# Performance work log

Measured on AMD Instinct MI355X. Metric: run time of the kernel, lower is better.

The kernel has to match this reference:

```python
import jax, jax.numpy as jnp
import numpy as np

_SHAPE = (4, 2, 8, 256, 513)  # N, 2(real/imag), C, T, F


def setup_inputs() -> dict:
    key = jax.random.key(0)
    k1, k2, k3 = jax.random.split(key, 3)
    return {
        "mixture": jax.random.normal(k1, _SHAPE, dtype=jnp.float32),
        "target": jax.random.normal(k2, _SHAPE, dtype=jnp.float32),
        "noise": jax.random.normal(k3, _SHAPE, dtype=jnp.float32),
        "ref_mic_idx": 0,
    }


def _to_complex(x):
    # (N, 2, C, T, F) real-imag stacked -> complex (N, C, T, F)
    return jax.lax.complex(x[:, 0], x[:, 1])


def _mean_spatial_cov(s):
    # s: complex (N, C, T, F) -> time-averaged covariance (N, F, C, C)
    N, C, T, F = s.shape
    sc = jnp.transpose(s, (0, 3, 2, 1))  # (N, F, T, C)
    # outer product V V^H summed over T, fused into one batched GEMM
    return jnp.einsum("nftc,nftd->nfcd", sc, jnp.conj(sc)) / T


def reference(mixture, target, noise, ref_mic_idx):
    y = _to_complex(mixture)  # (N, C, T, F)
    x = _to_complex(target)
    v = _to_complex(noise)
    N, C, T, F = y.shape

    phi_target = _mean_spatial_cov(x)  # (N, F, C, C)
    # diagonal loading: torch adds load to BOTH real and imag parts (RI dim broadcast)
    load = (0.001 / np.sqrt(2)) * (1.0 + 1.0j)
    phi_noise = _mean_spatial_cov(v) + jnp.asarray(load, dtype=y.dtype) * jnp.eye(C, dtype=y.dtype)

    G = jnp.linalg.inv(phi_noise) @ phi_target  # (N, F, C, C)
    l = jnp.trace(G, axis1=-2, axis2=-1)  # (N, F)
    # W = (1/l) * G @ e_ref  -> select column ref_mic_idx
    W = G[..., ref_mic_idx] / l[..., None]  # (N, F, C)

    # X_bf(n,t,f) = W^H y = sum_c conj(W)_{nfc} y_{nctf}
    X_bf = jnp.einsum("nfc,nctf->ntf", jnp.conj(W), y)  # (N, T, F)
    # restack real/imag and add singleton channel dim -> (N, 2, 1, T, F)
    out = jnp.stack([X_bf.real, X_bf.imag], axis=1)[:, :, None]
    return out
```

## Files before the change

kernel.cpp:

```cpp
#include <hip/hip_runtime.h>

#define Nn 4
#define Cc 8
#define Tt 256
#define Ff 513
#define TFs (Tt * Ff)
#define NPAIR 36

template <int G>
__device__ __forceinline__ void cov_body(const float* __restrict__ base,
                                         float* __restrict__ dst,
                                         int t0, int tchunk)
{
    constexpr int R2 = 7 - G;
    float ar[9], ai[9];
#pragma unroll
    for (int s = 0; s < 9; ++s) { ar[s] = 0.f; ai[s] = 0.f; }

    const float* bt = base + (size_t)t0 * Ff;
    for (int tt = 0; tt < tchunk; ++tt) {
        float re[8], im[8];
#pragma unroll
        for (int c = G; c < 8; ++c) {
            re[c] = bt[(size_t)c * TFs];
            im[c] = bt[(size_t)(Cc + c) * TFs];
        }
        int s = 0;
#pragma unroll
        for (int d = G; d < 8; ++d, ++s) {
            ar[s] += re[G] * re[d] + im[G] * im[d];
            ai[s] += im[G] * re[d] - re[G] * im[d];
        }
#pragma unroll
        for (int d = R2; d < 8; ++d, ++s) {
            ar[s] += re[R2] * re[d] + im[R2] * im[d];
            ai[s] += im[R2] * re[d] - re[R2] * im[d];
        }
        bt += Ff;
    }

    int s = 0;
#pragma unroll
    for (int d = G; d < 8; ++d, ++s) {
        const int p = G * 8 - G * (G - 1) / 2 + (d - G);
        dst[(size_t)(p * 2 + 0) * Ff] = ar[s];
        dst[(size_t)(p * 2 + 1) * Ff] = ai[s];
    }
#pragma unroll
    for (int d = R2; d < 8; ++d, ++s) {
        const int p = R2 * 8 - R2 * (R2 - 1) / 2 + (d - R2);
        dst[(size_t)(p * 2 + 0) * Ff] = ar[s];
        dst[(size_t)(p * 2 + 1) * Ff] = ai[s];
    }
}

__global__ __launch_bounds__(64) void cov_partial(
    const float* __restrict__ target, const float* __restrict__ noise,
    float* __restrict__ partial, int nchunk, int tchunk)
{
    int f = blockIdx.x * 64 + threadIdx.x;
    if (f >= Ff) return;
    int n = blockIdx.y;
    int z = blockIdx.z;
    int g = z & 3;
    int inp = (z >> 2) & 1;
    int chunk = z >> 3;

    const float* src = inp ? noise : target;
    const float* base = src + (size_t)n * 2 * Cc * TFs + f;
    float* dst = partial +
        ((((size_t)inp * Nn + n) * nchunk + chunk) * (NPAIR * 2)) * Ff + f;
    int t0 = chunk * tchunk;

    switch (g) {
        case 0: cov_body<0>(base, dst, t0, tchunk); break;
        case 1: cov_body<1>(base, dst, t0, tchunk); break;
        case 2: cov_body<2>(base, dst, t0, tchunk); break;
        default: cov_body<3>(base, dst, t0, tchunk); break;
    }
}

__global__ __launch_bounds__(128) void mvdr_weights(
    const float* __restrict__ partial, const int* __restrict__ ref_ptr,
    float2* __restrict__ wconj, int nchunk)
{
    int f = blockIdx.x;
    int n = blockIdx.y;
    int tid = threadIdx.x;

    __shared__ float covT[72], covN[72];
    __shared__ float2 A[8][16];
    __shared__ float2 PT[8][8];
    __shared__ float2 gcol[8], trp[8];
    __shared__ int piv;

    if (tid < 72) {
        float sT = 0.f, sN = 0.f;
        for (int ch = 0; ch < nchunk; ++ch) {
            size_t iT = ((((size_t)0 * Nn + n) * nchunk + ch) * 72 + tid) * Ff + f;
            size_t iN = ((((size_t)1 * Nn + n) * nchunk + ch) * 72 + tid) * Ff + f;
            sT += partial[iT];
            sN += partial[iN];
        }
        covT[tid] = sT;
        covN[tid] = sN;
    }
    __syncthreads();

    const float invT = 1.0f / (float)Tt;
    const float dl = 0.001f / 1.41421356237309515f;

    if (tid < 64) {
        int r = tid >> 3, c = tid & 7;
        int lo = r <= c ? r : c, hi = r <= c ? c : r;
        int p = lo * 8 - lo * (lo - 1) / 2 + (hi - lo);
        float pr = covN[2 * p] * invT, pi = covN[2 * p + 1] * invT;
        if (r > c) pi = -pi;
        if (r == c) { pr += dl; pi += dl; }
        A[r][c] = make_float2(pr, pi);
        A[r][8 + c] = make_float2(r == c ? 1.f : 0.f, 0.f);
        float qr = covT[2 * p] * invT, qi = covT[2 * p + 1] * invT;
        if (r > c) qi = -qi;
        PT[r][c] = make_float2(qr, qi);
    }
    __syncthreads();

    int r = tid >> 4, col = tid & 15;
    for (int k = 0; k < 8; ++k) {
        if (tid == 0) {
            int best = k;
            float bm = A[k][k].x * A[k][k].x + A[k][k].y * A[k][k].y;
            for (int j = k + 1; j < 8; ++j) {
                float m = A[j][k].x * A[j][k].x + A[j][k].y * A[j][k].y;
                if (m > bm) { bm = m; best = j; }
            }
            piv = best;
        }
        __syncthreads();
        int pv_row = piv;
        if (pv_row != k && tid < 16) {
            float2 tmp = A[k][tid]; A[k][tid] = A[pv_row][tid]; A[pv_row][tid] = tmp;
        }
        __syncthreads();
        if (tid < 16) {
            float2 pv = A[k][k];
            float d = pv.x * pv.x + pv.y * pv.y;
            float2 ip = make_float2(pv.x / d, -pv.y / d);
            float2 a = A[k][tid];
            A[k][tid] = make_float2(a.x * ip.x - a.y * ip.y,
                                    a.x * ip.y + a.y * ip.x);
        }
        __syncthreads();
        float2 factor = A[r][k];
        float2 akc = A[k][col];
        if (r != k) {
            float2 v = A[r][col];
            A[r][col] = make_float2(v.x - (factor.x * akc.x - factor.y * akc.y),
                                    v.y - (factor.x * akc.y + factor.y * akc.x));
        }
        __syncthreads();
    }

    int ref = *ref_ptr;
    if (tid < 8) {
        float2 g = make_float2(0.f, 0.f), tr = make_float2(0.f, 0.f);
#pragma unroll
        for (int d = 0; d < 8; ++d) {
            float2 iv = A[tid][8 + d];
            float2 b = PT[d][ref];
            g.x += iv.x * b.x - iv.y * b.y;
            g.y += iv.x * b.y + iv.y * b.x;
            float2 b2 = PT[d][tid];
            tr.x += iv.x * b2.x - iv.y * b2.y;
            tr.y += iv.x * b2.y + iv.y * b2.x;
        }
        gcol[tid] = g; trp[tid] = tr;
    }
    __syncthreads();
    if (tid < 8) {
        float lx = 0.f, ly = 0.f;
#pragma unroll
        for (int j = 0; j < 8; ++j) { lx += trp[j].x; ly += trp[j].y; }
        float den = lx * lx + ly * ly;
        float2 g = gcol[tid];
        float wx = (g.x * lx + g.y * ly) / den;
        float wy = (g.y * lx - g.x * ly) / den;
        wconj[((size_t)n * Ff + f) * 8 + tid] = make_float2(wx, -wy);
    }
}

__global__ __launch_bounds__(256) void beamform(
    const float* __restrict__ y, const float2* __restrict__ wconj,
    float* __restrict__ out)
{
    int idx = blockIdx.x * 256 + threadIdx.x;
    int n = idx / TFs;
    int rem = idx - n * TFs;
    int t = rem / Ff;
    int f = rem - t * Ff;

    size_t base_re = (size_t)n * 2 * Cc * TFs + (size_t)t * Ff + f;
    size_t base_im = base_re + (size_t)Cc * TFs;
    const float2* w = wconj + ((size_t)n * Ff + f) * 8;

    float xr = 0.f, xi = 0.f;
#pragma unroll
    for (int c = 0; c < Cc; ++c) {
        float yre = y[base_re + (size_t)c * TFs];
        float yim = y[base_im + (size_t)c * TFs];
        float2 wc = w[c];
        xr += wc.x * yre - wc.y * yim;
        xi += wc.x * yim + wc.y * yre;
    }
    size_t ob = (size_t)n * 2 * TFs + (size_t)t * Ff + f;
    out[ob] = xr;
    out[ob + TFs] = xi;
}

extern "C" void kernel_launch(void* const* d_in, const int* in_sizes, int n_in,
                              void* d_out, int out_size, void* d_ws, size_t ws_size,
                              hipStream_t stream) {
    const float* mixture = (const float*)d_in[0];
    const float* target  = (const float*)d_in[1];
    const float* noise   = (const float*)d_in[2];
    const int*   refp    = (const int*)d_in[3];
    float* out = (float*)d_out;

    const size_t wconj_bytes = (size_t)Nn * Ff * 8 * sizeof(float2);
    int nchunk = 8;
    while (nchunk > 1 &&
           (size_t)2 * Nn * nchunk * 72 * Ff * sizeof(float) + wconj_bytes > ws_size)
        nchunk >>= 1;
    int tchunk = Tt / nchunk;

    float*  partial = (float*)d_ws;
    float2* wconj = (float2*)((char*)d_ws +
                              (size_t)2 * Nn * nchunk * 72 * Ff * sizeof(float));

    cov_partial<<<dim3(9, Nn, nchunk * 8), 64, 0, stream>>>(
        target, noise, partial, nchunk, tchunk);
    mvdr_weights<<<dim3(Ff, Nn), 128, 0, stream>>>(partial, refp, wconj, nchunk);
    beamform<<<dim3((Nn * TFs) / 256), 256, 0, stream>>>(mixture, wconj, out);
}
```

Before: 162.2 us.

## Compute all covariance pairs per thread and solve MVDR with wavefront shuffles

The covariance kernel now has each thread accumulate all 36 channel pairs over a fixed 16-chunk time split, replacing the four-way pair split with duplicated loads. The MVDR weight kernel drops the shared-memory Gauss-Jordan with many barriers. It runs a single 64-lane wavefront that holds one matrix element per lane and uses shuffles for pivoting, elimination and the trace reduction, solving inv(Phi_N)·Phi_T directly. This cuts redundant global reads and synchronisation, at the cost of much higher register pressure in cov_partial, a workspace that no longer shrinks to fit ws_size, and twice as many partial sums to reduce.

New measurement: 170.8 us. 5.3% more time.

```diff
diff --git a/kernel.cpp b/kernel.cpp
--- a/kernel.cpp
+++ b/kernel.cpp
@@ -5,187 +5,136 @@
 #define Tt 256
 #define Ff 513
 #define TFs (Tt * Ff)
-#define NPAIR 36
-
-template <int G>
-__device__ __forceinline__ void cov_body(const float* __restrict__ base,
-                                         float* __restrict__ dst,
-                                         int t0, int tchunk)
-{
-    constexpr int R2 = 7 - G;
-    float ar[9], ai[9];
-#pragma unroll
-    for (int s = 0; s < 9; ++s) { ar[s] = 0.f; ai[s] = 0.f; }
-
-    const float* bt = base + (size_t)t0 * Ff;
-    for (int tt = 0; tt < tchunk; ++tt) {
-        float re[8], im[8];
-#pragma unroll
-        for (int c = G; c < 8; ++c) {
-            re[c] = bt[(size_t)c * TFs];
-            im[c] = bt[(size_t)(Cc + c) * TFs];
-        }
-        int s = 0;
-#pragma unroll
-        for (int d = G; d < 8; ++d, ++s) {
-            ar[s] += re[G] * re[d] + im[G] * im[d];
-            ai[s] += im[G] * re[d] - re[G] * im[d];
-        }
-#pragma unroll
-        for (int d = R2; d < 8; ++d, ++s) {
-            ar[s] += re[R2] * re[d] + im[R2] * im[d];
-            ai[s] += im[R2] * re[d] - re[R2] * im[d];
-        }
-        bt += Ff;
-    }
-
-    int s = 0;
-#pragma unroll
-    for (int d = G; d < 8; ++d, ++s) {
-        const int p = G * 8 - G * (G - 1) / 2 + (d - G);
-        dst[(size_t)(p * 2 + 0) * Ff] = ar[s];
-        dst[(size_t)(p * 2 + 1) * Ff] = ai[s];
-    }
-#pragma unroll
-    for (int d = R2; d < 8; ++d, ++s) {
-        const int p = R2 * 8 - R2 * (R2 - 1) / 2 + (d - R2);
-        dst[(size_t)(p * 2 + 0) * Ff] = ar[s];
-        dst[(size_t)(p * 2 + 1) * Ff] = ai[s];
-    }
-}
+#define NCHUNK 16
+#define TCHUNK (Tt / NCHUNK)
 
 __global__ __launch_bounds__(64) void cov_partial(
     const float* __restrict__ target, const float* __restrict__ noise,
-    float* __restrict__ partial, int nchunk, int tchunk)
+    float* __restrict__ partial)
 {
     int f = blockIdx.x * 64 + threadIdx.x;
     if (f >= Ff) return;
     int n = blockIdx.y;
     int z = blockIdx.z;
-    int g = z & 3;
-    int inp = (z >> 2) & 1;
-    int chunk = z >> 3;
+    int inp = z & 1;
+    int chunk = z >> 1;
 
     const float* src = inp ? noise : target;
-    const float* base = src + (size_t)n * 2 * Cc * TFs + f;
-    float* dst = partial +
-        ((((size_t)inp * Nn + n) * nchunk + chunk) * (NPAIR * 2)) * Ff + f;
-    int t0 = chunk * tchunk;
+    const float* bt = src + (size_t)n * 2 * Cc * TFs + (size_t)(chunk * TCHUNK) * Ff + f;
 
-    switch (g) {
-        case 0: cov_body<0>(base, dst, t0, tchunk); break;
-        case 1: cov_body<1>(base, dst, t0, tchunk); break;
-        case 2: cov_body<2>(base, dst, t0, tchunk); break;
-        default: cov_body<3>(base, dst, t0, tchunk); break;
+    float ar[36], ai[36];
+#pragma unroll
+    for (int p = 0; p < 36; ++p) { ar[p] = 0.f; ai[p] = 0.f; }
+
+#pragma unroll 2
+    for (int tt = 0; tt < TCHUNK; ++tt) {
+        float re[8], im[8];
+#pragma unroll
+        for (int c = 0; c < 8; ++c) {
+            re[c] = bt[(size_t)c * TFs];
+            im[c] = bt[(size_t)(Cc + c) * TFs];
+        }
+        int p = 0;
+#pragma unroll
+        for (int a = 0; a < 8; ++a) {
+#pragma unroll
+            for (int b = a; b < 8; ++b, ++p) {
+                ar[p] += re[a] * re[b] + im[a] * im[b];
+                if (a != b)
+                    ai[p] += im[a] * re[b] - re[a] * im[b];
+            }
+        }
+        bt += Ff;
+    }
+
+    float* dst = partial + (((size_t)inp * Nn + n) * NCHUNK + chunk) * 72 * (size_t)Ff + f;
+#pragma unroll
+    for (int p = 0; p < 36; ++p) {
+        dst[(size_t)(2 * p + 0) * Ff] = ar[p];
+        dst[(size_t)(2 * p + 1) * Ff] = ai[p];
     }
 }
 
-__global__ __launch_bounds__(128) void mvdr_weights(
+__global__ __launch_bounds__(64) void mvdr_weights(
     const float* __restrict__ partial, const int* __restrict__ ref_ptr,
-    float2* __restrict__ wconj, int nchunk)
+    float2* __restrict__ wconj)
 {
     int f = blockIdx.x;
     int n = blockIdx.y;
-    int tid = threadIdx.x;
+    int lane = threadIdx.x;
 
-    __shared__ float covT[72], covN[72];
-    __shared__ float2 A[8][16];
-    __shared__ float2 PT[8][8];
-    __shared__ float2 gcol[8], trp[8];
-    __shared__ int piv;
+    __shared__ float cov[144];
 
-    if (tid < 72) {
-        float sT = 0.f, sN = 0.f;
-        for (int ch = 0; ch < nchunk; ++ch) {
-            size_t iT = ((((size_t)0 * Nn + n) * nchunk + ch) * 72 + tid) * Ff + f;
-            size_t iN = ((((size_t)1 * Nn + n) * nchunk + ch) * 72 + tid) * Ff + f;
-            sT += partial[iT];
-            sN += partial[iN];
-        }
-        covT[tid] = sT;
-        covN[tid] = sN;
+    for (int comp = lane; comp < 144; comp += 64) {
+        int inp = comp >= 72;
+        int idx = inp ? comp - 72 : comp;
+        float s = 0.f;
+#pragma unroll
+        for (int ch = 0; ch < NCHUNK; ++ch)
+            s += partial[((((size_t)inp * Nn + n) * NCHUNK + ch) * 72 + idx) * (size_t)Ff + f];
+        cov[comp] = s;
     }
     __syncthreads();
 
+    int r = lane >> 3, c = lane & 7;
+    int lo = r < c ? r : c, hi = r < c ? c : r;
+    int p = lo * 8 - lo * (lo - 1) / 2 + (hi - lo);
     const float invT = 1.0f / (float)Tt;
     const float dl = 0.001f / 1.41421356237309515f;
+    float sgn = (r > c) ? -1.f : 1.f;
 
-    if (tid < 64) {
-        int r = tid >> 3, c = tid & 7;
-        int lo = r <= c ? r : c, hi = r <= c ? c : r;
-        int p = lo * 8 - lo * (lo - 1) / 2 + (hi - lo);
-        float pr = covN[2 * p] * invT, pi = covN[2 * p + 1] * invT;
-        if (r > c) pi = -pi;
-        if (r == c) { pr += dl; pi += dl; }
-        A[r][c] = make_float2(pr, pi);
-        A[r][8 + c] = make_float2(r == c ? 1.f : 0.f, 0.f);
-        float qr = covT[2 * p] * invT, qi = covT[2 * p + 1] * invT;
-        if (r > c) qi = -qi;
-        PT[r][c] = make_float2(qr, qi);
+    float2 a = make_float2(cov[72 + 2 * p] * invT, sgn * cov[72 + 2 * p + 1] * invT);
+    float2 b = make_float2(cov[2 * p] * invT,      sgn * cov[2 * p + 1] * invT);
+    if (r == c) { a.x += dl; a.y += dl; }
+
+    for (int k = 0; k < 8; ++k) {
+        float mag = (c == k && r >= k) ? (a.x * a.x + a.y * a.y) : -1.f;
+        int midx = r;
+#pragma unroll
+        for (int st = 8; st < 64; st <<= 1) {
+            float om = __shfl_xor(mag, st, 64);
+            int   oi = __shfl_xor(midx, st, 64);
+            if (om > mag) { mag = om; midx = oi; }
+        }
+        int piv = __shfl(midx, k, 64);
+
+        int srcr = (r == k) ? piv : ((r == piv) ? k : r);
+        int src = srcr * 8 + c;
+        a.x = __shfl(a.x, src, 64); a.y = __shfl(a.y, src, 64);
+        b.x = __shfl(b.x, src, 64); b.y = __shfl(b.y, src, 64);
+
+        float pvx = __shfl(a.x, k * 8 + k, 64), pvy = __shfl(a.y, k * 8 + k, 64);
+        float d = pvx * pvx + pvy * pvy;
+        float ipx = pvx / d, ipy = -pvy / d;
+        if (r == k) {
+            float2 t = a;
+            a = make_float2(t.x * ipx - t.y * ipy, t.x * ipy + t.y * ipx);
+            t = b;
+            b = make_float2(t.x * ipx - t.y * ipy, t.x * ipy + t.y * ipx);
+        }
+
+        float rax = __shfl(a.x, k * 8 + c, 64), ray = __shfl(a.y, k * 8 + c, 64);
+        float rbx = __shfl(b.x, k * 8 + c, 64), rby = __shfl(b.y, k * 8 + c, 64);
+        float fx  = __shfl(a.x, r * 8 + k, 64), fy  = __shfl(a.y, r * 8 + k, 64);
+        if (r != k) {
+            a.x -= fx * rax - fy * ray;  a.y -= fx * ray + fy * rax;
+            b.x -= fx * rbx - fy * rby;  b.y -= fx * rby + fy * rbx;
+        }
     }
-    __syncthreads();
 
-    int r = tid >> 4, col = tid & 15;
-    for (int k = 0; k < 8; ++k) {
-        if (tid == 0) {
-            int best = k;
-            float bm = A[k][k].x * A[k][k].x + A[k][k].y * A[k][k].y;
-            for (int j = k + 1; j < 8; ++j) {
-                float m = A[j][k].x * A[j][k].x + A[j][k].y * A[j][k].y;
-                if (m > bm) { bm = m; best = j; }
-            }
-            piv = best;
-        }
-        __syncthreads();
-        int pv_row = piv;
-        if (pv_row != k && tid < 16) {
-            float2 tmp = A[k][tid]; A[k][tid] = A[pv_row][tid]; A[pv_row][tid] = tmp;
-        }
-        __syncthreads();
-        if (tid < 16) {
-            float2 pv = A[k][k];
-            float d = pv.x * pv.x + pv.y * pv.y;
-            float2 ip = make_float2(pv.x / d, -pv.y / d);
-            float2 a = A[k][tid];
-            A[k][tid] = make_float2(a.x * ip.x - a.y * ip.y,
-                                    a.x * ip.y + a.y * ip.x);
-        }
-        __syncthreads();
-        float2 factor = A[r][k];
-        float2 akc = A[k][col];
-        if (r != k) {
-            float2 v = A[r][col];
-            A[r][col] = make_float2(v.x - (factor.x * akc.x - factor.y * akc.y),
-                                    v.y - (factor.x * akc.y + factor.y * akc.x));
-        }
-        __syncthreads();
+    float tx = (r == c) ? b.x : 0.f, ty = (r == c) ? b.y : 0.f;
+#pragma unroll
+    for (int st = 1; st < 64; st <<= 1) {
+        tx += __shfl_xor(tx, st, 64);
+        ty += __shfl_xor(ty, st, 64);
     }
 
     int ref = *ref_ptr;
-    if (tid < 8) {
-        float2 g = make_float2(0.f, 0.f), tr = make_float2(0.f, 0.f);
-#pragma unroll
-        for (int d = 0; d < 8; ++d) {
-            float2 iv = A[tid][8 + d];
-            float2 b = PT[d][ref];
-            g.x += iv.x * b.x - iv.y * b.y;
-            g.y += iv.x * b.y + iv.y * b.x;
-            float2 b2 = PT[d][tid];
-            tr.x += iv.x * b2.x - iv.y * b2.y;
-            tr.y += iv.x * b2.y + iv.y * b2.x;
-        }
-        gcol[tid] = g; trp[tid] = tr;
-    }
-    __syncthreads();
-    if (tid < 8) {
-        float lx = 0.f, ly = 0.f;
-#pragma unroll
-        for (int j = 0; j < 8; ++j) { lx += trp[j].x; ly += trp[j].y; }
-        float den = lx * lx + ly * ly;
-        float2 g = gcol[tid];
-        float wx = (g.x * lx + g.y * ly) / den;
-        float wy = (g.y * lx - g.x * ly) / den;
-        wconj[((size_t)n * Ff + f) * 8 + tid] = make_float2(wx, -wy);
+    if (c == ref) {
+        float den = tx * tx + ty * ty;
+        float wx = (b.x * tx + b.y * ty) / den;
+        float wy = (b.y * tx - b.x * ty) / den;
+        wconj[((size_t)n * Ff + f) * 8 + r] = make_float2(wx, -wy);
     }
 }
 
@@ -226,19 +175,11 @@
     const int*   refp    = (const int*)d_in[3];
     float* out = (float*)d_out;
 
-    const size_t wconj_bytes = (size_t)Nn * Ff * 8 * sizeof(float2);
-    int nchunk = 8;
-    while (nchunk > 1 &&
-           (size_t)2 * Nn * nchunk * 72 * Ff * sizeof(float) + wconj_bytes > ws_size)
-        nchunk >>= 1;
-    int tchunk = Tt / nchunk;
-
     float*  partial = (float*)d_ws;
     float2* wconj = (float2*)((char*)d_ws +
-                              (size_t)2 * Nn * nchunk * 72 * Ff * sizeof(float));
+                              (size_t)2 * Nn * NCHUNK * 72 * Ff * sizeof(float));
 
-    cov_partial<<<dim3(9, Nn, nchunk * 8), 64, 0, stream>>>(
-        target, noise, partial, nchunk, tchunk);
-    mvdr_weights<<<dim3(Ff, Nn), 128, 0, stream>>>(partial, refp, wconj, nchunk);
+    cov_partial<<<dim3(9, Nn, NCHUNK * 2), 64, 0, stream>>>(target, noise, partial);
+    mvdr_weights<<<dim3(Ff, Nn), 64, 0, stream>>>(partial, refp, wconj);
     beamform<<<dim3((Nn * TFs) / 256), 256, 0, stream>>>(mixture, wconj, out);
 }
```
